# Optimization experiments

Hardware: AMD Instinct MI355X
Metric: run time of the kernel (lower is better)

## Reference

```python
import jax, jax.numpy as jnp
import numpy as np

B, S, F, H = 4, 8192, 1024, 16
D = F // H  # k_dim = 64
EPS = 1e-6


def setup_inputs() -> dict:
    rng = jax.random.key(0)
    ks = jax.random.split(rng, 6)
    # xavier-normal-ish scale for square (F, F) kernels
    w_std = float(np.sqrt(2.0 / (F + F)))
    return {
        "query": jax.random.normal(ks[0], (B, S, F), jnp.float32),
        "key": jax.random.normal(ks[1], (B, S, F), jnp.float32),
        "value": jax.random.normal(ks[2], (B, S, F), jnp.float32),
        "Wq": jax.random.normal(ks[3], (F, F), jnp.float32) * w_std,
        "Wk": jax.random.normal(ks[4], (F, F), jnp.float32) * w_std,
        "Wv": jax.random.normal(ks[5], (F, F), jnp.float32) * w_std,
        # per-head LayerNorm params for K and V (galerkin branch): (H, D)
        "ln_k_scale": jnp.ones((H, D), jnp.float32),
        "ln_k_bias": jnp.zeros((H, D), jnp.float32),
        "ln_v_scale": jnp.ones((H, D), jnp.float32),
        "ln_v_bias": jnp.zeros((H, D), jnp.float32),
    }


def _per_head_layernorm(x, scale, bias):
    # x: (B, H, N, D); scale/bias: (H, D) -> broadcast per head
    mu = jnp.mean(x, axis=-1, keepdims=True)
    var = jnp.var(x, axis=-1, keepdims=True)
    xn = (x - mu) * jax.lax.rsqrt(var + EPS)
    return xn * scale[None, :, None, :] + bias[None, :, None, :]


def reference(query, key, value, Wq, Wk, Wv, ln_k_scale, ln_k_bias, ln_v_scale, ln_v_bias):
    # QKV projections (no bias), then the module's raw contiguous reshape
    # (B, S, F) -> (B, H, S, D)  [NOT a head transpose -- faithful to source]
    q = jnp.matmul(query, Wq).reshape(B, H, -1, D)
    k = jnp.matmul(key, Wk).reshape(B, H, -1, D)
    v = jnp.matmul(value, Wv).reshape(B, H, -1, D)
    # galerkin: per-head LayerNorm on K and V only
    k = _per_head_layernorm(k, ln_k_scale, ln_k_bias)
    v = _per_head_layernorm(v, ln_v_scale, ln_v_bias)
    # linear (galerkin) attention: p_attn = K^T V / seq_len; out = Q p_attn
    seq_len = v.shape[-2]
    p_attn = jnp.einsum('bhnd,bhne->bhde', k, v) / seq_len  # (B, H, D, D)
    x = jnp.einsum('bhnd,bhde->bhne', q, p_attn)            # (B, H, N, D)
    att_output = x.reshape(B, -1, H * D)                    # (B, S, F)
    return (att_output, p_attn)
```

## Files before the change

kernel.cpp:

```cpp
#include <hip/hip_runtime.h>
#include <hip/hip_bf16.h>
#include <stdint.h>

#define DEVI __device__ __forceinline__

typedef __attribute__((ext_vector_type(8))) short bf16x8;
typedef __attribute__((ext_vector_type(4))) float f32x4;

static constexpr int Bb = 4, Ss = 8192, Ff = 1024, Hh = 16, Dd = 64;
static constexpr int Mm = Bb * Ss;
static constexpr int Kk = Ff;
static constexpr int PROJ_ELEMS = Mm * Ff;

DEVI ushort f2bf(float f) {
  uint32_t u = __builtin_bit_cast(uint32_t, f);
  u += 0x7fffu + ((u >> 16) & 1u);
  return (ushort)(u >> 16);
}
DEVI float bf2f(ushort u) { return __builtin_bit_cast(float, (uint32_t)u << 16); }

DEVI uint32_t pack2(float a, float b) {
  return (uint32_t)f2bf(a) | ((uint32_t)f2bf(b) << 16);
}

DEVI void async16(void* lds, const void* g) {
  __builtin_amdgcn_global_load_lds((const __attribute__((address_space(1))) void*)g,
                                   (__attribute__((address_space(3))) void*)lds,
                                   16, 0, 0);
}

__global__ __launch_bounds__(256) void cast_kernel(const float* __restrict__ q,
                                                   const float* __restrict__ k,
                                                   const float* __restrict__ v,
                                                   ushort* __restrict__ abf) {
  const int b = blockIdx.x;
  const int proj = b >> 11;
  const float* src = (proj == 0) ? q : ((proj == 1) ? k : v);
  ushort* dst = abf + (size_t)proj * PROJ_ELEMS;
  const int tid0 = (b & 2047) * 256 + threadIdx.x;
#pragma unroll
  for (int p = 0; p < 8; ++p) {
    const size_t i = ((size_t)p * 524288 + (size_t)tid0) * 8;
    const float4 f0 = *(const float4*)(src + i);
    const float4 f1 = *(const float4*)(src + i + 4);
    uint4 o;
    o.x = pack2(f0.x, f0.y);
    o.y = pack2(f0.z, f0.w);
    o.z = pack2(f1.x, f1.y);
    o.w = pack2(f1.z, f1.w);
    *(uint4*)(dst + i) = o;
  }
}

__global__ __launch_bounds__(256) void wt_kernel(const float* __restrict__ Wq,
                                                 const float* __restrict__ Wk,
                                                 const float* __restrict__ Wv,
                                                 ushort* __restrict__ wt) {
  __shared__ float tile[64][65];
  int b = blockIdx.x;
  const int w = b >> 8; b &= 255;
  const int kt = b >> 4, nt = b & 15;
  const float* Wsrc = (w == 0) ? Wq : ((w == 1) ? Wk : Wv);
  ushort* dst = wt + (size_t)w * 1024 * 1024;
  const int t = threadIdx.x;
  const int r = t >> 6, c = t & 63;
#pragma unroll
  for (int i = 0; i < 16; i++) {
    const int kk = kt * 64 + r + i * 4;
    tile[r + i * 4][c] = Wsrc[(size_t)kk * 1024 + nt * 64 + c];
  }
  __syncthreads();
#pragma unroll
  for (int i = 0; i < 16; i++) {
    const int nn = nt * 64 + r + i * 4;
    dst[(size_t)nn * 1024 + kt * 64 + c] = f2bf(tile[c][r + i * 4]);
  }
}

__global__ __launch_bounds__(256, 4) void gemm_qkv_kernel(
    const ushort* __restrict__ Abf, const ushort* __restrict__ Wt,
    ushort* __restrict__ Cout,
    const float* __restrict__ ksc, const float* __restrict__ kbi,
    const float* __restrict__ vsc, const float* __restrict__ vbi) {
  __shared__ __align__(16) ushort As[128][64];
  __shared__ __align__(16) ushort Bs[128][64];

  const int bx0 = blockIdx.x;
  const int bx = (bx0 & 7) * 768 + (bx0 >> 3);
  const int proj = bx >> 11;
  const int t2 = bx & 2047;
  const int mt = t2 >> 3;
  const int nt = t2 & 7;
  const ushort* A = Abf + (size_t)proj * PROJ_ELEMS;
  const ushort* Bw = Wt + (size_t)proj * 1024 * 1024;
  ushort* C = Cout + (size_t)proj * PROJ_ELEMS;
  const int m0 = mt * 128, n0 = nt * 128;
  const int tid = threadIdx.x;
  const int lane = tid & 63;
  const int wave = tid >> 6;
  const int wy = wave >> 1, wx = wave & 1;

  const f32x4 fzero = {0.0f, 0.0f, 0.0f, 0.0f};
  f32x4 acc[4][4];
#pragma unroll
  for (int i = 0; i < 4; i++)
#pragma unroll
    for (int j = 0; j < 4; j++) acc[i][j] = fzero;

  const int srow = lane >> 3;
  const int scol = (lane & 7) * 8;

  for (int k0 = 0; k0 < Kk; k0 += 64) {
#pragma unroll
    for (int j = 0; j < 4; j++) {
      const int seg = wave * 4 + j;
      async16(&As[seg * 8][0], A + (size_t)(m0 + seg * 8 + srow) * Kk + k0 + scol);
      async16(&Bs[seg * 8][0], Bw + (size_t)(n0 + seg * 8 + srow) * Kk + k0 + scol);
    }
    __syncthreads();
#pragma unroll
    for (int ks = 0; ks < 2; ks++) {
      bf16x8 af[4], bv[4];
#pragma unroll
      for (int i = 0; i < 4; i++)
        af[i] = *(const bf16x8*)&As[wy * 64 + i * 16 + (lane & 15)][ks * 32 + (lane >> 4) * 8];
#pragma unroll
      for (int j = 0; j < 4; j++)
        bv[j] = *(const bf16x8*)&Bs[wx * 64 + j * 16 + (lane & 15)][ks * 32 + (lane >> 4) * 8];
#pragma unroll
      for (int i = 0; i < 4; i++)
#pragma unroll
        for (int j = 0; j < 4; j++)
          acc[i][j] = __builtin_amdgcn_mfma_f32_16x16x32_bf16(af[i], bv[j], acc[i][j], 0, 0, 0);
    }
    __syncthreads();
  }

  if (proj == 0) {
#pragma unroll
    for (int i = 0; i < 4; i++) {
      const int rbase = m0 + wy * 64 + i * 16 + (lane >> 4) * 4;
#pragma unroll
      for (int j = 0; j < 4; j++) {
        const int col = n0 + wx * 64 + j * 16 + (lane & 15);
#pragma unroll
        for (int r = 0; r < 4; r++)
          C[(size_t)(rbase + r) * 1024 + col] = f2bf(acc[i][j][r]);
      }
    }
  } else {
    const float* sc = (proj == 1) ? ksc : vsc;
    const float* bi = (proj == 1) ? kbi : vbi;
    const int h = (m0 >> 9) & 15;
    float scv[4], biv[4];
#pragma unroll
    for (int j = 0; j < 4; j++) {
      const int d = j * 16 + (lane & 15);
      scv[j] = sc[h * 64 + d];
      biv[j] = bi[h * 64 + d];
    }
#pragma unroll
    for (int i = 0; i < 4; i++) {
      const int rbase = m0 + wy * 64 + i * 16 + (lane >> 4) * 4;
#pragma unroll
      for (int r = 0; r < 4; r++) {
        float s = 0.f, sq = 0.f;
#pragma unroll
        for (int j = 0; j < 4; j++) {
          const float x = acc[i][j][r];
          s += x;
          sq += x * x;
        }
        s += __shfl_xor(s, 1); s += __shfl_xor(s, 2);
        s += __shfl_xor(s, 4); s += __shfl_xor(s, 8);
        sq += __shfl_xor(sq, 1); sq += __shfl_xor(sq, 2);
        sq += __shfl_xor(sq, 4); sq += __shfl_xor(sq, 8);
        const float mean = s * (1.0f / 64.0f);
        const float var = sq * (1.0f / 64.0f) - mean * mean;
        const float rs = rsqrtf(var + 1e-6f);
#pragma unroll
        for (int j = 0; j < 4; j++) {
          const int col = n0 + wx * 64 + j * 16 + (lane & 15);
          C[(size_t)(rbase + r) * 1024 + col] =
              f2bf((acc[i][j][r] - mean) * rs * scv[j] + biv[j]);
        }
      }
    }
  }
}

__global__ __launch_bounds__(256, 3) void gemm_qkv_legacy(
    const float* __restrict__ Aq, const float* __restrict__ Ak,
    const float* __restrict__ Av, const ushort* __restrict__ Wt,
    ushort* __restrict__ Cout,
    const float* __restrict__ ksc, const float* __restrict__ kbi,
    const float* __restrict__ vsc, const float* __restrict__ vbi) {
  __shared__ __align__(16) ushort As[128][64];
  __shared__ __align__(16) ushort Bs[128][64];

  const int bx0 = blockIdx.x;
  const int bx = (bx0 & 7) * 768 + (bx0 >> 3);
  const int proj = bx >> 11;
  const int t2 = bx & 2047;
  const int mt = t2 >> 3;
  const int nt = t2 & 7;
  const float* A = (proj == 0) ? Aq : ((proj == 1) ? Ak : Av);
  const ushort* Bw = Wt + (size_t)proj * 1024 * 1024;
  ushort* C = Cout + (size_t)proj * PROJ_ELEMS;
  const int m0 = mt * 128, n0 = nt * 128;
  const int tid = threadIdx.x;
  const int lane = tid & 63;
  const int wave = tid >> 6;
  const int wy = wave >> 1, wx = wave & 1;
  const int ar = tid >> 3;
  const int ac = (tid & 7) * 8;
  const float* Abase = A + (size_t)m0 * Kk;

  const f32x4 fzero = {0.0f, 0.0f, 0.0f, 0.0f};
  f32x4 acc[4][4];
#pragma unroll
  for (int i = 0; i < 4; i++)
#pragma unroll
    for (int j = 0; j < 4; j++) acc[i][j] = fzero;

  for (int k0 = 0; k0 < Kk; k0 += 64) {
#pragma unroll
    for (int j = 0; j < 4; j++) {
      const int seg = wave * 4 + j;
      const int brow = seg * 8 + (lane >> 3);
      const int bcol = (lane & 7) * 8;
      async16(&Bs[seg * 8][0], Bw + (size_t)(n0 + brow) * Kk + k0 + bcol);
    }
#pragma unroll
    for (int i = 0; i < 4; i++) {
      const int row = ar + i * 32;
      const float* src = Abase + (size_t)row * Kk + k0 + ac;
      const float4 f0 = *(const float4*)src;
      const float4 f1 = *(const float4*)(src + 4);
      uint4 v;
      v.x = pack2(f0.x, f0.y);
      v.y = pack2(f0.z, f0.w);
      v.z = pack2(f1.x, f1.y);
      v.w = pack2(f1.z, f1.w);
      *(uint4*)&As[row][ac] = v;
    }
    __syncthreads();
#pragma unroll
    for (int ks = 0; ks < 2; ks++) {
      bf16x8 af[4], bv[4];
#pragma unroll
      for (int i = 0; i < 4; i++)
        af[i] = *(const bf16x8*)&As[wy * 64 + i * 16 + (lane & 15)][ks * 32 + (lane >> 4) * 8];
#pragma unroll
      for (int j = 0; j < 4; j++)
        bv[j] = *(const bf16x8*)&Bs[wx * 64 + j * 16 + (lane & 15)][ks * 32 + (lane >> 4) * 8];
#pragma unroll
      for (int i = 0; i < 4; i++)
#pragma unroll
        for (int j = 0; j < 4; j++)
          acc[i][j] = __builtin_amdgcn_mfma_f32_16x16x32_bf16(af[i], bv[j], acc[i][j], 0, 0, 0);
    }
    __syncthreads();
  }

  if (proj == 0) {
#pragma unroll
    for (int i = 0; i < 4; i++) {
      const int rbase = m0 + wy * 64 + i * 16 + (lane >> 4) * 4;
#pragma unroll
      for (int j = 0; j < 4; j++) {
        const int col = n0 + wx * 64 + j * 16 + (lane & 15);
#pragma unroll
        for (int r = 0; r < 4; r++)
          C[(size_t)(rbase + r) * 1024 + col] = f2bf(acc[i][j][r]);
      }
    }
  } else {
    const float* sc = (proj == 1) ? ksc : vsc;
    const float* bi = (proj == 1) ? kbi : vbi;
    const int h = (m0 >> 9) & 15;
    float scv[4], biv[4];
#pragma unroll
    for (int j = 0; j < 4; j++) {
      const int d = j * 16 + (lane & 15);
      scv[j] = sc[h * 64 + d];
      biv[j] = bi[h * 64 + d];
    }
#pragma unroll
    for (int i = 0; i < 4; i++) {
      const int rbase = m0 + wy * 64 + i * 16 + (lane >> 4) * 4;
#pragma unroll
      for (int r = 0; r < 4; r++) {
        float s = 0.f, sq = 0.f;
#pragma unroll
        for (int j = 0; j < 4; j++) {
          const float x = acc[i][j][r];
          s += x;
          sq += x * x;
        }
        s += __shfl_xor(s, 1); s += __shfl_xor(s, 2);
        s += __shfl_xor(s, 4); s += __shfl_xor(s, 8);
        sq += __shfl_xor(sq, 1); sq += __shfl_xor(sq, 2);
        sq += __shfl_xor(sq, 4); sq += __shfl_xor(sq, 8);
        const float mean = s * (1.0f / 64.0f);
        const float var = sq * (1.0f / 64.0f) - mean * mean;
        const float rs = rsqrtf(var + 1e-6f);
#pragma unroll
        for (int j = 0; j < 4; j++) {
          const int col = n0 + wx * 64 + j * 16 + (lane & 15);
          C[(size_t)(rbase + r) * 1024 + col] =
              f2bf((acc[i][j][r] - mean) * rs * scv[j] + biv[j]);
        }
      }
    }
  }
}

__global__ __launch_bounds__(256) void pattn_kernel(const ushort* __restrict__ kp,
                                                    const ushort* __restrict__ vp,
                                                    float* __restrict__ praw) {
  __shared__ __align__(16) ushort kT[64][72];
  __shared__ __align__(16) ushort vT[64][72];
  const int bh = blockIdx.x >> 4;
  const int nc = blockIdx.x & 15;
  const ushort* kb = kp + ((size_t)bh << 19) + (size_t)nc * 32768;
  const ushort* vb = vp + ((size_t)bh << 19) + (size_t)nc * 32768;
  const int tid = threadIdx.x;
  const int lane = tid & 63;
  const int wave = tid >> 6;
  const int d0 = wave * 16;
  const f32x4 fzero = {0.0f, 0.0f, 0.0f, 0.0f};
  f32x4 acc[4];
#pragma unroll
  for (int e = 0; e < 4; e++) acc[e] = fzero;

  for (int c = 0; c < 8; c++) {
    const ushort* kc = kb + c * 4096;
    const ushort* vc = vb + c * 4096;
    const uint4 ka = *(const uint4*)(kc + (size_t)lane * 64 + d0);
    const uint4 ka2 = *(const uint4*)(kc + (size_t)lane * 64 + d0 + 8);
    const uint4 va = *(const uint4*)(vc + (size_t)lane * 64 + d0);
    const uint4 va2 = *(const uint4*)(vc + (size_t)lane * 64 + d0 + 8);
    __syncthreads();
    const uint32_t* kw = (const uint32_t*)&ka;
    const uint32_t* kw2 = (const uint32_t*)&ka2;
    const uint32_t* vw = (const uint32_t*)&va;
    const uint32_t* vw2 = (const uint32_t*)&va2;
#pragma unroll
    for (int j = 0; j < 4; j++) {
      kT[d0 + 2 * j][lane] = (ushort)(kw[j] & 0xffffu);
      kT[d0 + 2 * j + 1][lane] = (ushort)(kw[j] >> 16);
      kT[d0 + 8 + 2 * j][lane] = (ushort)(kw2[j] & 0xffffu);
      kT[d0 + 8 + 2 * j + 1][lane] = (ushort)(kw2[j] >> 16);
      vT[d0 + 2 * j][lane] = (ushort)(vw[j] & 0xffffu);
      vT[d0 + 2 * j + 1][lane] = (ushort)(vw[j] >> 16);
      vT[d0 + 8 + 2 * j][lane] = (ushort)(vw2[j] & 0xffffu);
      vT[d0 + 8 + 2 * j + 1][lane] = (ushort)(vw2[j] >> 16);
    }
    __syncthreads();
#pragma unroll
    for (int ks = 0; ks < 2; ks++) {
      const bf16x8 af = *(const bf16x8*)&kT[wave * 16 + (lane & 15)][ks * 32 + (lane >> 4) * 8];
#pragma unroll
      for (int e = 0; e < 4; e++) {
        const bf16x8 bv = *(const bf16x8*)&vT[e * 16 + (lane & 15)][ks * 32 + (lane >> 4) * 8];
        acc[e] = __builtin_amdgcn_mfma_f32_16x16x32_bf16(af, bv, acc[e], 0, 0, 0);
      }
    }
  }
#pragma unroll
  for (int e = 0; e < 4; e++)
#pragma unroll
    for (int r = 0; r < 4; r++) {
      const int drow = wave * 16 + (lane >> 4) * 4 + r;
      const int ecol = e * 16 + (lane & 15);
      atomicAdd(&praw[(size_t)bh * 4096 + drow * 64 + ecol], acc[e][r]);
    }
}

__global__ __launch_bounds__(256) void scalep_kernel(const float* __restrict__ praw,
                                                     float* __restrict__ pout) {
  const int i = blockIdx.x * 256 + threadIdx.x;
  pout[i] = praw[i] * (1.0f / 8192.0f);
}

__global__ __launch_bounds__(256) void outgemm_kernel(const ushort* __restrict__ qp,
                                                      const float* __restrict__ praw,
                                                      float* __restrict__ xout) {
  __shared__ __align__(16) ushort pT[64][72];
  const int bh = blockIdx.x >> 5;
  const int mc = blockIdx.x & 31;
  const ushort* qb = qp + ((size_t)bh << 19) + (size_t)mc * 256 * 64;
  float* ob = xout + ((size_t)bh << 19) + (size_t)mc * 256 * 64;
  const float* pb = praw + (size_t)bh * 4096;
  const int tid = threadIdx.x;
  const int lane = tid & 63;
  const int wave = tid >> 6;
  for (int i = tid; i < 4096; i += 256) {
    const int d = i >> 6, e = i & 63;
    pT[e][d] = f2bf(pb[i] * (1.0f / 8192.0f));
  }
  __syncthreads();
  bf16x8 bv[4][2];
#pragma unroll
  for (int e = 0; e < 4; e++)
#pragma unroll
    for (int ks = 0; ks < 2; ks++)
      bv[e][ks] = *(const bf16x8*)&pT[e * 16 + (lane & 15)][ks * 32 + (lane >> 4) * 8];
  const f32x4 fzero = {0.0f, 0.0f, 0.0f, 0.0f};
  for (int it = 0; it < 4; it++) {
    const int rbase = it * 64 + wave * 16;
    const ushort* qrow = qb + (size_t)rbase * 64;
    const bf16x8 a0 = *(const bf16x8*)(qrow + (size_t)(lane & 15) * 64 + (lane >> 4) * 8);
    const bf16x8 a1 = *(const bf16x8*)(qrow + (size_t)(lane & 15) * 64 + (lane >> 4) * 8 + 32);
    f32x4 acc[4];
#pragma unroll
    for (int e = 0; e < 4; e++) acc[e] = fzero;
#pragma unroll
    for (int e = 0; e < 4; e++) {
      acc[e] = __builtin_amdgcn_mfma_f32_16x16x32_bf16(a0, bv[e][0], acc[e], 0, 0, 0);
      acc[e] = __builtin_amdgcn_mfma_f32_16x16x32_bf16(a1, bv[e][1], acc[e], 0, 0, 0);
    }
#pragma unroll
    for (int e = 0; e < 4; e++)
#pragma unroll
      for (int r = 0; r < 4; r++)
        ob[(size_t)(rbase + (lane >> 4) * 4 + r) * 64 + e * 16 + (lane & 15)] = acc[e][r];
  }
}

extern "C" void kernel_launch(void* const* d_in, const int* in_sizes, int n_in,
                              void* d_out, int out_size, void* d_ws, size_t ws_size,
                              hipStream_t stream) {
  const float* q_in = (const float*)d_in[0];
  const float* k_in = (const float*)d_in[1];
  const float* v_in = (const float*)d_in[2];
  const float* Wq = (const float*)d_in[3];
  const float* Wk = (const float*)d_in[4];
  const float* Wv = (const float*)d_in[5];
  const float* ksc = (const float*)d_in[6];
  const float* kbi = (const float*)d_in[7];
  const float* vsc = (const float*)d_in[8];
  const float* vbi = (const float*)d_in[9];

  float* att = (float*)d_out;
  float* pout = att + (size_t)PROJ_ELEMS;

  const size_t need_new = (size_t)3 * PROJ_ELEMS * 2 * 2
                        + (size_t)3 * 1024 * 1024 * 2
                        + (size_t)262144 * 4;
  if (ws_size >= need_new) {
    ushort* a_bf = (ushort*)d_ws;
    ushort* q_proj = a_bf + (size_t)3 * PROJ_ELEMS;
    ushort* k_proj = q_proj + (size_t)PROJ_ELEMS;
    ushort* v_proj = k_proj + (size_t)PROJ_ELEMS;
    ushort* wtb = v_proj + (size_t)PROJ_ELEMS;
    float* praw = (float*)(wtb + (size_t)3 * 1024 * 1024);

    wt_kernel<<<768, 256, 0, stream>>>(Wq, Wk, Wv, wtb);
    cast_kernel<<<6144, 256, 0, stream>>>(q_in, k_in, v_in, a_bf);
    gemm_qkv_kernel<<<6144, 256, 0, stream>>>(a_bf, wtb, q_proj, ksc, kbi, vsc, vbi);
    (void)hipMemsetAsync(praw, 0, (size_t)Bb * Hh * 64 * 64 * sizeof(float), stream);
    pattn_kernel<<<1024, 256, 0, stream>>>(k_proj, v_proj, praw);
    scalep_kernel<<<1024, 256, 0, stream>>>(praw, pout);
    outgemm_kernel<<<2048, 256, 0, stream>>>(q_proj, praw, att);
  } else {
    ushort* q_proj = (ushort*)d_ws;
    ushort* k_proj = q_proj + (size_t)PROJ_ELEMS;
    ushort* v_proj = k_proj + (size_t)PROJ_ELEMS;
    ushort* wtb = v_proj + (size_t)PROJ_ELEMS;
    float* praw = (float*)(wtb + (size_t)3 * 1024 * 1024);

    wt_kernel<<<768, 256, 0, stream>>>(Wq, Wk, Wv, wtb);
    gemm_qkv_legacy<<<6144, 256, 0, stream>>>(q_in, k_in, v_in, wtb, q_proj,
                                              ksc, kbi, vsc, vbi);
    (void)hipMemsetAsync(praw, 0, (size_t)Bb * Hh * 64 * 64 * sizeof(float), stream);
    pattn_kernel<<<1024, 256, 0, stream>>>(k_proj, v_proj, praw);
    scalep_kernel<<<1024, 256, 0, stream>>>(praw, pout);
    outgemm_kernel<<<2048, 256, 0, stream>>>(q_proj, praw, att);
  }
}
```

Measured before the change: 784.7 us.

## Swizzle GEMM LDS tiles, prefetch in pattn, replace atomics with partial-sum reduce

The QKV GEMM now XOR-swizzles the 16-byte column chunks of its A/B shared-memory tiles to cut LDS bank conflicts on fragment reads. It also raises wave priority around the MFMA block. The pattn kernel register-prefetches the next K/V chunk while it writes the current one to LDS. Its atomic accumulation into a zeroed buffer is replaced by plain stores of 16 partial sums, reduced and scaled by a new kernel, which removes the memset and the atomic contention at the cost of extra workspace and traffic. In the fallback path the legacy GEMM writes projections the pattn kernel reads, but the larger partial buffer may exceed the smaller workspace.

```diff
diff --git a/kernel.cpp b/kernel.cpp
--- a/kernel.cpp
+++ b/kernel.cpp
@@ -108,30 +108,41 @@
     for (int j = 0; j < 4; j++) acc[i][j] = fzero;
 
   const int srow = lane >> 3;
-  const int scol = (lane & 7) * 8;
+  const int schunk = lane & 7;
+  const int q4 = lane >> 4;
 
   for (int k0 = 0; k0 < Kk; k0 += 64) {
 #pragma unroll
     for (int j = 0; j < 4; j++) {
       const int seg = wave * 4 + j;
-      async16(&As[seg * 8][0], A + (size_t)(m0 + seg * 8 + srow) * Kk + k0 + scol);
-      async16(&Bs[seg * 8][0], Bw + (size_t)(n0 + seg * 8 + srow) * Kk + k0 + scol);
+      const int row = seg * 8 + srow;
+      const int sw = (schunk ^ ((row >> 1) & 7)) * 8;
+      async16(&As[seg * 8][0], A + (size_t)(m0 + row) * Kk + k0 + sw);
+      async16(&Bs[seg * 8][0], Bw + (size_t)(n0 + row) * Kk + k0 + sw);
     }
     __syncthreads();
 #pragma unroll
     for (int ks = 0; ks < 2; ks++) {
       bf16x8 af[4], bv[4];
 #pragma unroll
-      for (int i = 0; i < 4; i++)
-        af[i] = *(const bf16x8*)&As[wy * 64 + i * 16 + (lane & 15)][ks * 32 + (lane >> 4) * 8];
-#pragma unroll
-      for (int j = 0; j < 4; j++)
-        bv[j] = *(const bf16x8*)&Bs[wx * 64 + j * 16 + (lane & 15)][ks * 32 + (lane >> 4) * 8];
+      for (int i = 0; i < 4; i++) {
+        const int row = wy * 64 + i * 16 + (lane & 15);
+        const int pc = ((ks * 4 + q4) ^ ((row >> 1) & 7)) * 8;
+        af[i] = *(const bf16x8*)&As[row][pc];
+      }
+#pragma unroll
+      for (int j = 0; j < 4; j++) {
+        const int row = wx * 64 + j * 16 + (lane & 15);
+        const int pc = ((ks * 4 + q4) ^ ((row >> 1) & 7)) * 8;
+        bv[j] = *(const bf16x8*)&Bs[row][pc];
+      }
+      __builtin_amdgcn_s_setprio(1);
 #pragma unroll
       for (int i = 0; i < 4; i++)
 #pragma unroll
         for (int j = 0; j < 4; j++)
           acc[i][j] = __builtin_amdgcn_mfma_f32_16x16x32_bf16(af[i], bv[j], acc[i][j], 0, 0, 0);
+      __builtin_amdgcn_s_setprio(0);
     }
     __syncthreads();
   }
@@ -318,7 +329,7 @@
 
 __global__ __launch_bounds__(256) void pattn_kernel(const ushort* __restrict__ kp,
                                                     const ushort* __restrict__ vp,
-                                                    float* __restrict__ praw) {
+                                                    float* __restrict__ praw2) {
   __shared__ __align__(16) ushort kT[64][72];
   __shared__ __align__(16) ushort vT[64][72];
   const int bh = blockIdx.x >> 4;
@@ -334,13 +345,13 @@
 #pragma unroll
   for (int e = 0; e < 4; e++) acc[e] = fzero;
 
+  const size_t loff = (size_t)lane * 64 + d0;
+  uint4 ka  = *(const uint4*)(kb + loff);
+  uint4 ka2 = *(const uint4*)(kb + loff + 8);
+  uint4 va  = *(const uint4*)(vb + loff);
+  uint4 va2 = *(const uint4*)(vb + loff + 8);
+
   for (int c = 0; c < 8; c++) {
-    const ushort* kc = kb + c * 4096;
-    const ushort* vc = vb + c * 4096;
-    const uint4 ka = *(const uint4*)(kc + (size_t)lane * 64 + d0);
-    const uint4 ka2 = *(const uint4*)(kc + (size_t)lane * 64 + d0 + 8);
-    const uint4 va = *(const uint4*)(vc + (size_t)lane * 64 + d0);
-    const uint4 va2 = *(const uint4*)(vc + (size_t)lane * 64 + d0 + 8);
     __syncthreads();
     const uint32_t* kw = (const uint32_t*)&ka;
     const uint32_t* kw2 = (const uint32_t*)&ka2;
@@ -357,6 +368,13 @@
       vT[d0 + 8 + 2 * j][lane] = (ushort)(vw2[j] & 0xffffu);
       vT[d0 + 8 + 2 * j + 1][lane] = (ushort)(vw2[j] >> 16);
     }
+    if (c < 7) {
+      const size_t noff = loff + (size_t)(c + 1) * 4096;
+      ka  = *(const uint4*)(kb + noff);
+      ka2 = *(const uint4*)(kb + noff + 8);
+      va  = *(const uint4*)(vb + noff);
+      va2 = *(const uint4*)(vb + noff + 8);
+    }
     __syncthreads();
 #pragma unroll
     for (int ks = 0; ks < 2; ks++) {
@@ -368,37 +386,41 @@
       }
     }
   }
+  float* out = praw2 + ((size_t)nc * 64 + bh) * 4096;
 #pragma unroll
   for (int e = 0; e < 4; e++)
 #pragma unroll
     for (int r = 0; r < 4; r++) {
       const int drow = wave * 16 + (lane >> 4) * 4 + r;
       const int ecol = e * 16 + (lane & 15);
-      atomicAdd(&praw[(size_t)bh * 4096 + drow * 64 + ecol], acc[e][r]);
-    }
-}
-
-__global__ __launch_bounds__(256) void scalep_kernel(const float* __restrict__ praw,
-                                                     float* __restrict__ pout) {
+      out[drow * 64 + ecol] = acc[e][r];
+    }
+}
+
+__global__ __launch_bounds__(256) void preduce_kernel(const float* __restrict__ praw2,
+                                                      float* __restrict__ pout) {
   const int i = blockIdx.x * 256 + threadIdx.x;
-  pout[i] = praw[i] * (1.0f / 8192.0f);
+  float s = 0.f;
+#pragma unroll
+  for (int p = 0; p < 16; ++p) s += praw2[(size_t)p * 262144 + i];
+  pout[i] = s * (1.0f / 8192.0f);
 }
 
 __global__ __launch_bounds__(256) void outgemm_kernel(const ushort* __restrict__ qp,
-                                                      const float* __restrict__ praw,
+                                                      const float* __restrict__ pout,
                                                       float* __restrict__ xout) {
   __shared__ __align__(16) ushort pT[64][72];
   const int bh = blockIdx.x >> 5;
   const int mc = blockIdx.x & 31;
   const ushort* qb = qp + ((size_t)bh << 19) + (size_t)mc * 256 * 64;
   float* ob = xout + ((size_t)bh << 19) + (size_t)mc * 256 * 64;
-  const float* pb = praw + (size_t)bh * 4096;
+  const float* pb = pout + (size_t)bh * 4096;
   const int tid = threadIdx.x;
   const int lane = tid & 63;
   const int wave = tid >> 6;
   for (int i = tid; i < 4096; i += 256) {
     const int d = i >> 6, e = i & 63;
-    pT[e][d] = f2bf(pb[i] * (1.0f / 8192.0f));
+    pT[e][d] = f2bf(pb[i]);
   }
   __syncthreads();
   bf16x8 bv[4][2];
@@ -448,35 +470,33 @@
 
   const size_t need_new = (size_t)3 * PROJ_ELEMS * 2 * 2
                         + (size_t)3 * 1024 * 1024 * 2
-                        + (size_t)262144 * 4;
+                        + (size_t)16 * 262144 * 4;
   if (ws_size >= need_new) {
     ushort* a_bf = (ushort*)d_ws;
     ushort* q_proj = a_bf + (size_t)3 * PROJ_ELEMS;
     ushort* k_proj = q_proj + (size_t)PROJ_ELEMS;
     ushort* v_proj = k_proj + (size_t)PROJ_ELEMS;
     ushort* wtb = v_proj + (size_t)PROJ_ELEMS;
-    float* praw = (float*)(wtb + (size_t)3 * 1024 * 1024);
+    float* praw2 = (float*)(wtb + (size_t)3 * 1024 * 1024);
 
     wt_kernel<<<768, 256, 0, stream>>>(Wq, Wk, Wv, wtb);
     cast_kernel<<<6144, 256, 0, stream>>>(q_in, k_in, v_in, a_bf);
     gemm_qkv_kernel<<<6144, 256, 0, stream>>>(a_bf, wtb, q_proj, ksc, kbi, vsc, vbi);
-    (void)hipMemsetAsync(praw, 0, (size_t)Bb * Hh * 64 * 64 * sizeof(float), stream);
-    pattn_kernel<<<1024, 256, 0, stream>>>(k_proj, v_proj, praw);
-    scalep_kernel<<<1024, 256, 0, stream>>>(praw, pout);
-    outgemm_kernel<<<2048, 256, 0, stream>>>(q_proj, praw, att);
+    pattn_kernel<<<1024, 256, 0, stream>>>(k_proj, v_proj, praw2);
+    preduce_kernel<<<1024, 256, 0, stream>>>(praw2, pout);
+    outgemm_kernel<<<2048, 256, 0, stream>>>(q_proj, pout, att);
   } else {
     ushort* q_proj = (ushort*)d_ws;
     ushort* k_proj = q_proj + (size_t)PROJ_ELEMS;
     ushort* v_proj = k_proj + (size_t)PROJ_ELEMS;
     ushort* wtb = v_proj + (size_t)PROJ_ELEMS;
-    float* praw = (float*)(wtb + (size_t)3 * 1024 * 1024);
+    float* praw2 = (float*)(wtb + (size_t)3 * 1024 * 1024);
 
     wt_kernel<<<768, 256, 0, stream>>>(Wq, Wk, Wv, wtb);
     gemm_qkv_legacy<<<6144, 256, 0, stream>>>(q_in, k_in, v_in, wtb, q_proj,
                                               ksc, kbi, vsc, vbi);
-    (void)hipMemsetAsync(praw, 0, (size_t)Bb * Hh * 64 * 64 * sizeof(float), stream);
-    pattn_kernel<<<1024, 256, 0, stream>>>(k_proj, v_proj, praw);
-    scalep_kernel<<<1024, 256, 0, stream>>>(praw, pout);
-    outgemm_kernel<<<2048, 256, 0, stream>>>(q_proj, praw, att);
-  }
-}
+    pattn_kernel<<<1024, 256, 0, stream>>>(k_proj, v_proj, praw2);
+    preduce_kernel<<<1024, 256, 0, stream>>>(praw2, pout);
+    outgemm_kernel<<<2048, 256, 0, stream>>>(q_proj, pout, att);
+  }
+}
```

After: 745.2 us. 1.05x faster.
